# Kernel tuning notes

Hardware: AMD Instinct MI355X
Metric: run time of the kernel (lower is better)

## Reference

```python
import jax, jax.numpy as jnp
import numpy as np

B, N, F_IN, H, OUT = 64, 1024, 195, 128, 64
K1, K2 = N // 2, N // 4  # ceil(0.5*N), ceil(0.5*K1)
EPS = 1e-5


def setup_inputs() -> dict:
    key = jax.random.key(0)
    ks = jax.random.split(key, 16)
    rn = lambda k, s: jax.random.normal(k, s, dtype=jnp.float32) * 0.1
    inp = {
        "input": jax.random.normal(ks[0], (B, N, F_IN), dtype=jnp.float32),
        # SAGEConv1 (195->128): lin_l (neighbors, w/ bias), lin_r (root, no bias)
        "W1l": rn(ks[1], (H, F_IN)), "b1l": jnp.zeros((H,), jnp.float32),
        "W1r": rn(ks[2], (H, F_IN)),
        # SAGPooling1 GNN = GraphConv(128->1): lin_rel (sum aggr, w/ bias), lin_root (no bias)
        "Wp1_rel": rn(ks[3], (1, H)), "bp1_rel": jnp.zeros((1,), jnp.float32),
        "Wp1_root": rn(ks[4], (1, H)),
        # SAGEConv2 (128->64)
        "W2l": rn(ks[5], (OUT, H)), "b2l": jnp.zeros((OUT,), jnp.float32),
        "W2r": rn(ks[6], (OUT, H)),
        # SAGPooling2 GNN = GraphConv(64->1)
        "Wp2_rel": rn(ks[7], (1, OUT)), "bp2_rel": jnp.zeros((1,), jnp.float32),
        "Wp2_root": rn(ks[8], (1, OUT)),
        # MLP head
        "fc1_w": rn(ks[9], (512, OUT)), "fc1_b": jnp.zeros((512,), jnp.float32),
        "bn1_g": jnp.ones((512,), jnp.float32), "bn1_b": jnp.zeros((512,), jnp.float32),
        "bn1_m": jnp.zeros((512,), jnp.float32), "bn1_v": jnp.ones((512,), jnp.float32),
        "fc2_w": rn(ks[10], (256, 512)), "fc2_b": jnp.zeros((256,), jnp.float32),
        "bn2_g": jnp.ones((256,), jnp.float32), "bn2_b": jnp.zeros((256,), jnp.float32),
        "bn2_m": jnp.zeros((256,), jnp.float32), "bn2_v": jnp.ones((256,), jnp.float32),
        "fc3_w": rn(ks[11], (2, 256)), "fc3_b": jnp.zeros((2,), jnp.float32),
    }
    return inp


def _corr_adj(x):
    # Pearson corrcoef over rows of x [B,N,F] -> boolean adjacency [B,N,N] (corr > 0.5)
    xc = x - x.mean(axis=-1, keepdims=True)
    cov = jnp.einsum("bnf,bmf->bnm", xc, xc)
    d = jnp.sqrt(jnp.clip(jnp.einsum("bnnf->bn", cov[..., None] * 0 + 0) + jnp.diagonal(cov, axis1=1, axis2=2), 1e-12))
    corr = cov / (d[:, :, None] * d[:, None, :])
    return (corr > 0.5).astype(x.dtype)  # symmetric, includes self-loops


def _sage(x, A, Wl, bl, Wr):
    # PyG SAGEConv: lin_l(mean_{j in N(i)} x_j) + lin_r(x_i)
    deg = A.sum(axis=-1, keepdims=True)
    agg = jnp.einsum("bnm,bmf->bnf", A, x) / jnp.maximum(deg, 1.0)
    return jnp.einsum("bnf,hf->bnh", agg, Wl) + bl + jnp.einsum("bnf,hf->bnh", x, Wr)


def _sagpool(x, A, Wrel, brel, Wroot, k):
    # score via GraphConv (sum aggr): lin_rel(sum_j x_j) + lin_root(x_i)
    agg = jnp.einsum("bnm,bmf->bnf", A, x)
    score = (jnp.einsum("bnf,of->bno", agg, Wrel) + brel
             + jnp.einsum("bnf,of->bno", x, Wroot))[..., 0]  # [B,N]
    top_s, idx = jax.lax.top_k(score, k)  # per-graph top-k nodes
    x_new = jnp.take_along_axis(x, idx[:, :, None], axis=1) * jnp.tanh(top_s)[:, :, None]
    A_new = jnp.take_along_axis(A, idx[:, :, None], axis=1)
    A_new = jnp.take_along_axis(A_new, idx[:, None, :], axis=2)
    return x_new, A_new


def _bn_eval(x, g, b, m, v):
    return g * (x - m) * jax.lax.rsqrt(v + EPS) + b


def reference(input, W1l, b1l, W1r, Wp1_rel, bp1_rel, Wp1_root,
              W2l, b2l, W2r, Wp2_rel, bp2_rel, Wp2_root,
              fc1_w, fc1_b, bn1_g, bn1_b, bn1_m, bn1_v,
              fc2_w, fc2_b, bn2_g, bn2_b, bn2_m, bn2_v,
              fc3_w, fc3_b):
    A = _corr_adj(input)                                   # [B,N,N]
    x = jax.nn.relu(_sage(input, A, W1l, b1l, W1r))        # [B,N,128]
    x, A = _sagpool(x, A, Wp1_rel, bp1_rel, Wp1_root, K1)  # [B,K1,128]
    x = jax.nn.relu(_sage(x, A, W2l, b2l, W2r))            # [B,K1,64]
    x, A = _sagpool(x, A, Wp2_rel, bp2_rel, Wp2_root, K2)  # [B,K2,64]
    x = x.mean(axis=1)                                     # global mean pool -> [B,64]
    x = _bn_eval(jax.nn.relu(x @ fc1_w.T + fc1_b), bn1_g, bn1_b, bn1_m, bn1_v)
    x = _bn_eval(jax.nn.relu(x @ fc2_w.T + fc2_b), bn2_g, bn2_b, bn2_m, bn2_v)
    x = x @ fc3_w.T + fc3_b
    return jax.nn.softmax(x, axis=1)
```

## Files before the change

### kernel.cpp

```cpp
#include <hip/hip_runtime.h>
#include <hip/hip_fp8.h>
#include <cstdint>


typedef __bf16 bf16x8 __attribute__((ext_vector_type(8)));
typedef float  floatx4 __attribute__((ext_vector_type(4)));

#define MFMA_BF16(a, b, c) __builtin_amdgcn_mfma_f32_16x16x32_bf16((a), (b), (c), 0, 0, 0)
#define MFMA_FP8(a, b, c)  __builtin_amdgcn_mfma_f32_16x16x32_fp8_fp8((a), (b), (c), 0, 0, 0)

typedef __attribute__((address_space(1))) const void as1_cvoid;
typedef __attribute__((address_space(3))) void as3_void;
static __device__ __forceinline__ void gl16(const void* g, void* l) {
  __builtin_amdgcn_global_load_lds((as1_cvoid*)g, (as3_void*)l, 16, 0, 0);
}

static constexpr int BATCH = 64, NNODE = 1024, FIN = 195, FPAD = 224;
static constexpr int HD = 128, OD = 64, KP1 = 512, KP2 = 256;

static constexpr size_t OFF_GHI   = 0;
static constexpr size_t OFF_GLO   = 8388608;
static constexpr size_t OFF_A1B   = 16777216;
static constexpr size_t OFF_YR2   = 18874368;
static constexpr size_t OFF_X2    = 35651584;
static constexpr size_t OFF_XHI   = 0;
static constexpr size_t OFF_XLO   = 29360128;
static constexpr size_t OFF_ABITS = 58720256;
static constexpr size_t OFF_X1    = 67108864;
static constexpr size_t OFF_P1    = 100663296;
static constexpr size_t OFF_Q1    = OFF_P1 + 262144;
static constexpr size_t OFF_IDX1  = OFF_Q1 + 262144;
static constexpr size_t OFF_GATE1 = OFF_IDX1 + 131072;
static constexpr size_t OFF_P2    = OFF_GATE1 + 131072;
static constexpr size_t OFF_Q2    = OFF_P2 + 131072;
static constexpr size_t OFF_W1HI  = OFF_Q2 + 131072;
static constexpr size_t OFF_W1LO  = OFF_W1HI + 114688;
static constexpr size_t OFF_W2HI  = OFF_W1LO + 114688;
static constexpr size_t OFF_W2LO  = OFF_W2HI + 32768;
static constexpr size_t OFF_FC1T  = OFF_W2LO + 32768;
static constexpr size_t OFF_FC2T  = OFF_FC1T + 131072;
static constexpr size_t OFF_XHAT  = 102760448;
static constexpr size_t OFF_YR1   = 102760448 + 16777216;

static __device__ __forceinline__ unsigned char to_fp8(float v) {
  __hip_fp8_e4m3 q(v);
  return *(unsigned char*)&q;
}

__global__ __launch_bounds__(256) void prep_pack_kernel(
    const float* __restrict__ x, __bf16* __restrict__ xhi,
    __bf16* __restrict__ xlo, unsigned char* __restrict__ xhat8,
    const float* __restrict__ W1l, const float* __restrict__ W1r,
    __bf16* __restrict__ hi1, __bf16* __restrict__ lo1,
    const float* __restrict__ W2l, const float* __restrict__ W2r,
    __bf16* __restrict__ hi2, __bf16* __restrict__ lo2,
    const float* __restrict__ fc1w, float* __restrict__ fc1t,
    const float* __restrict__ fc2w, float* __restrict__ fc2t) {
  int bid = blockIdx.x;
  if (bid < 16384) {
    int row  = bid * 4 + (threadIdx.x >> 6);
    int lane = threadIdx.x & 63;
    const float* xr = x + (long)row * FIN;
    int k0 = lane * 4;
    float v[4];
#pragma unroll
    for (int i = 0; i < 4; ++i) v[i] = (k0 + i < FIN) ? xr[k0 + i] : 0.f;
    float s = v[0] + v[1] + v[2] + v[3];
#pragma unroll
    for (int o = 32; o; o >>= 1) s += __shfl_xor(s, o);
    float mean = s * (1.f / (float)FIN);
    float c[4], ss = 0.f;
#pragma unroll
    for (int i = 0; i < 4; ++i) {
      c[i] = (k0 + i < FIN) ? (v[i] - mean) : 0.f;
      ss += c[i] * c[i];
    }
#pragma unroll
    for (int o = 32; o; o >>= 1) ss += __shfl_xor(ss, o);
    float inv = rsqrtf(fmaxf(ss, 1e-12f));
    if (k0 < FPAD) {
      __bf16 hi4[4], lo4[4];
      unsigned char h8[4];
#pragma unroll
      for (int i = 0; i < 4; ++i) {
        float xv = (k0 + i < FIN) ? v[i] : 0.f;
        __bf16 h = (__bf16)xv;
        hi4[i] = h;
        lo4[i] = (__bf16)(xv - (float)h);
        h8[i] = to_fp8(c[i] * inv);
      }
      long base = (long)row * FPAD + k0;
      *(uint2*)&xhi[base] = *(const uint2*)hi4;
      *(uint2*)&xlo[base] = *(const uint2*)lo4;
      *(unsigned int*)&xhat8[base] = *(const unsigned int*)h8;
    }
  } else if (bid < 16384 + 224) {
    int idx = (bid - 16384) * 256 + threadIdx.x;
    int h = idx / FPAD, k = idx % FPAD;
    float v = 0.f;
    if (k < FIN) v = (h < HD) ? W1l[h * FIN + k] : W1r[(h - HD) * FIN + k];
    __bf16 a = (__bf16)v;
    hi1[idx] = a;
    lo1[idx] = (__bf16)(v - (float)a);
  } else if (bid < 16672) {
    int idx = (bid - 16384 - 224) * 256 + threadIdx.x;
    int h = idx / HD, k = idx % HD;
    float v = (h < OD) ? W2l[h * HD + k] : W2r[(h - OD) * HD + k];
    __bf16 a = (__bf16)v;
    hi2[idx] = a;
    lo2[idx] = (__bf16)(v - (float)a);
  } else if (bid < 16800) {
    int idx = (bid - 16672) * 256 + threadIdx.x;
    int o = idx & 511, j = idx >> 9;
    fc1t[idx] = fc1w[o * 64 + j];
  } else {
    int idx = (bid - 16800) * 256 + threadIdx.x;
    int o = idx & 255, j = idx >> 8;
    fc2t[idx] = fc2w[o * 512 + j];
  }
}

static constexpr int CKB = 48;
__global__ __launch_bounds__(256, 3) void corr_gemm1_kernel(
    const unsigned char* __restrict__ xhat8, unsigned short* __restrict__ Abits,
    const __bf16* __restrict__ Ahi, const __bf16* __restrict__ Alo,
    const __bf16* __restrict__ Bhi, const __bf16* __restrict__ Blo,
    float* __restrict__ C) {
  __shared__ __align__(16) char pool[32768];
  int bid = blockIdx.x;
  int t = threadIdx.x;
  int lane = t & 63, wave = t >> 6;
  int wi = (wave >> 1) * 64, wj = (wave & 1) * 64;
  int lr = lane & 15;
  if (bid < 2304) {
    unsigned char* sI = (unsigned char*)pool;
    unsigned char* sJ = (unsigned char*)pool + 2 * 128 * CKB;
    int xcd = bid & 7;
    int m = bid >> 3;
    int b = xcd + ((m & 7) << 3);
    int rem = m >> 3, bi = 0;
    while (rem >= 8 - bi) { rem -= 8 - bi; ++bi; }
    int bj = bi + rem;
    int i0 = bi * 128, j0 = bj * 128;
    const unsigned char* Xb = xhat8 + (long)b * NNODE * FPAD;
    int lk8 = (lane >> 4) * 8;
    int strow = t & 127;
    int sbuf = t >> 7;
    const unsigned char* src = Xb + (long)((sbuf ? j0 : i0) + strow) * FPAD;
    unsigned char* dst0 = (sbuf ? sJ : sI) + strow * CKB;
    floatx4 zero = {0.f, 0.f, 0.f, 0.f};
    floatx4 acc[4][4];
#pragma unroll
    for (int i = 0; i < 4; ++i)
#pragma unroll
      for (int j = 0; j < 4; ++j) acc[i][j] = zero;
    {
      uint4 u0 = *(const uint4*)(src);
      uint4 u1 = *(const uint4*)(src + 16);
      *(uint4*)(dst0)      = u0;
      *(uint4*)(dst0 + 16) = u1;
    }
    __syncthreads();
    for (int kk = 0; kk < 7; ++kk) {
      int cur = kk & 1;
      uint4 u0, u1;
      if (kk < 6) {
        const unsigned char* s2 = src + (kk + 1) * 32;
        u0 = *(const uint4*)(s2);
        u1 = *(const uint4*)(s2 + 16);
      }
      const unsigned char* rI = sI + cur * (128 * CKB);
      const unsigned char* rJ = sJ + cur * (128 * CKB);
      long long af[4], bf[4];
#pragma unroll
      for (int tt = 0; tt < 4; ++tt) {
        af[tt] = *(const long long*)&rI[(wi + tt * 16 + lr) * CKB + lk8];
        bf[tt] = *(const long long*)&rJ[(wj + tt * 16 + lr) * CKB + lk8];
      }
#pragma unroll
      for (int ti = 0; ti < 4; ++ti)
#pragma unroll
        for (int tj = 0; tj < 4; ++tj)
          acc[ti][tj] = MFMA_FP8(af[ti], bf[tj], acc[ti][tj]);
      if (kk < 6) {
        unsigned char* d = dst0 + (cur ? 0 : 128 * CKB);
        *(uint4*)(d)      = u0;
        *(uint4*)(d + 16) = u1;
        __syncthreads();
      }
    }
#pragma unroll
    for (int ti = 0; ti < 4; ++ti)
#pragma unroll
      for (int tj = 0; tj < 4; ++tj) {
        floatx4 a = acc[ti][tj];
        unsigned long long mr[4];
        mr[0] = __ballot(a[0] > 0.5f);
        mr[1] = __ballot(a[1] > 0.5f);
        mr[2] = __ballot(a[2] > 0.5f);
        mr[3] = __ballot(a[3] > 0.5f);
        if (lane < 16) {
          unsigned long long mm = mr[lane & 3];
          unsigned short piece = (unsigned short)(mm >> ((lane >> 2) * 16));
          int grow = i0 + wi + ti * 16 + lane;
          int gcol = (j0 + wj + tj * 16) >> 4;
          Abits[((long)b * NNODE + grow) * 64 + gcol] = piece;
          if (bi != bj) {
            unsigned int tp = 0;
#pragma unroll
            for (int tb = 0; tb < 16; ++tb)
              tp |= (unsigned int)((mr[tb & 3] >> ((tb >> 2) * 16 + lane)) & 1ULL) << tb;
            int grow2 = j0 + wj + tj * 16 + lane;
            int gcol2 = (i0 + wi + ti * 16) >> 4;
            Abits[((long)b * NNODE + grow2) * 64 + gcol2] = (unsigned short)tp;
          }
        }
      }
  } else {
    constexpr int K = 224;
    constexpr int ldc = 256;
    int gid = bid - 2304;
    int xcd = gid & 7;
    int q = gid >> 3;
    int col = q & 1;
    int mrow = (xcd << 6) + (q >> 1);
    __bf16* sAh = (__bf16*)pool;
    __bf16* sAl = (__bf16*)(pool + 8192);
    __bf16* sBh = (__bf16*)(pool + 16384);
    __bf16* sBl = (__bf16*)(pool + 24576);
    long row0 = (long)mrow * 128;
    int col0 = col * 128;
    int lk2 = (lane >> 4) * 16;
    int lk2s = lk2 ^ (((lr >> 1) & 3) << 4);
    int sr = t >> 2;
    int scb = (((t & 3) ^ ((sr >> 1) & 3)) << 4);
    const char* gA0 = (const char*)Ahi + (row0 + sr) * (long)K * 2 + scb;
    const char* gA1 = (const char*)Alo + (row0 + sr) * (long)K * 2 + scb;
    const char* gB0 = (const char*)Bhi + (long)(col0 + sr) * K * 2 + scb;
    const char* gB1 = (const char*)Blo + (long)(col0 + sr) * K * 2 + scb;
    constexpr long rstep = 64L * K * 2;
    char* lAh = (char*)sAh + (wave << 10);
    char* lAl = (char*)sAl + (wave << 10);
    char* lBh = (char*)sBh + (wave << 10);
    char* lBl = (char*)sBl + (wave << 10);
    floatx4 zero = {0.f, 0.f, 0.f, 0.f};
    floatx4 acc[4][4];
#pragma unroll
    for (int i = 0; i < 4; ++i)
#pragma unroll
      for (int j = 0; j < 4; ++j) acc[i][j] = zero;
    for (int kk = 0; kk < (K >> 5); ++kk) {
      __syncthreads();
      gl16(gA0, lAh); gl16(gA0 + rstep, lAh + 4096);
      gl16(gA1, lAl); gl16(gA1 + rstep, lAl + 4096);
      gl16(gB0, lBh); gl16(gB0 + rstep, lBh + 4096);
      gl16(gB1, lBl); gl16(gB1 + rstep, lBl + 4096);
      gA0 += 64; gA1 += 64; gB0 += 64; gB1 += 64;
      __syncthreads();
      bf16x8 bh[4], bl[4];
#pragma unroll
      for (int tj = 0; tj < 4; ++tj) {
        bh[tj] = *(const bf16x8*)((const char*)sBh + (wj + tj * 16 + lr) * 64 + lk2s);
        bl[tj] = *(const bf16x8*)((const char*)sBl + (wj + tj * 16 + lr) * 64 + lk2s);
      }
#pragma unroll
      for (int ti = 0; ti < 4; ++ti) {
        bf16x8 ah = *(const bf16x8*)((const char*)sAh + (wi + ti * 16 + lr) * 64 + lk2s);
        bf16x8 al = *(const bf16x8*)((const char*)sAl + (wi + ti * 16 + lr) * 64 + lk2s);
#pragma unroll
        for (int tj = 0; tj < 4; ++tj) acc[ti][tj] = MFMA_BF16(ah, bh[tj], acc[ti][tj]);
#pragma unroll
        for (int tj = 0; tj < 4; ++tj) acc[ti][tj] = MFMA_BF16(ah, bl[tj], acc[ti][tj]);
#pragma unroll
        for (int tj = 0; tj < 4; ++tj) acc[ti][tj] = MFMA_BF16(al, bh[tj], acc[ti][tj]);
      }
    }
#pragma unroll
    for (int ti = 0; ti < 4; ++ti)
#pragma unroll
      for (int tj = 0; tj < 4; ++tj)
#pragma unroll
        for (int rr = 0; rr < 4; ++rr) {
          long grow = row0 + wi + ti * 16 + (lane >> 4) * 4 + rr;
          int gcol = col0 + wj + tj * 16 + (lane & 15);
          C[grow * ldc + gcol] = acc[ti][tj][rr];
        }
  }
}

template <int K, int NCOL>
__global__ __launch_bounds__(256, 3) void gemm_split_kernel(
    const __bf16* __restrict__ Ahi, const __bf16* __restrict__ Alo,
    const __bf16* __restrict__ Bhi, const __bf16* __restrict__ Blo,
    float* __restrict__ C) {
  constexpr int ldc = NCOL * 128;
  int bid = blockIdx.x;
  int mrow, col;
  if (NCOL == 2) {
    int xcd = bid & 7;
    int q = bid >> 3;
    col = q & 1;
    mrow = (xcd << 6) + (q >> 1);
  } else {
    mrow = bid;
    col = 0;
  }
  __shared__ __align__(16) __bf16 sAh[128 * 32];
  __shared__ __align__(16) __bf16 sAl[128 * 32];
  __shared__ __align__(16) __bf16 sBh[128 * 32];
  __shared__ __align__(16) __bf16 sBl[128 * 32];
  long row0 = (long)mrow * 128;
  int col0 = col * 128;
  int t = threadIdx.x;
  int lane = t & 63, wave = t >> 6;
  int wi = (wave >> 1) * 64, wj = (wave & 1) * 64;
  int lr = lane & 15, lk2 = (lane >> 4) * 16;
  int lk2s = lk2 ^ (((lr >> 1) & 3) << 4);
  int sr = t >> 2;
  int scb = (((t & 3) ^ ((sr >> 1) & 3)) << 4);
  const char* gA0 = (const char*)Ahi + (row0 + sr) * (long)K * 2 + scb;
  const char* gA1 = (const char*)Alo + (row0 + sr) * (long)K * 2 + scb;
  const char* gB0 = (const char*)Bhi + (long)(col0 + sr) * K * 2 + scb;
  const char* gB1 = (const char*)Blo + (long)(col0 + sr) * K * 2 + scb;
  constexpr long rstep = 64L * K * 2;
  char* lAh = (char*)sAh + (wave << 10);
  char* lAl = (char*)sAl + (wave << 10);
  char* lBh = (char*)sBh + (wave << 10);
  char* lBl = (char*)sBl + (wave << 10);
  floatx4 zero = {0.f, 0.f, 0.f, 0.f};
  floatx4 acc[4][4];
#pragma unroll
  for (int i = 0; i < 4; ++i)
#pragma unroll
    for (int j = 0; j < 4; ++j) acc[i][j] = zero;
  for (int kk = 0; kk < (K >> 5); ++kk) {
    __syncthreads();
    gl16(gA0, lAh); gl16(gA0 + rstep, lAh + 4096);
    gl16(gA1, lAl); gl16(gA1 + rstep, lAl + 4096);
    gl16(gB0, lBh); gl16(gB0 + rstep, lBh + 4096);
    gl16(gB1, lBl); gl16(gB1 + rstep, lBl + 4096);
    gA0 += 64; gA1 += 64; gB0 += 64; gB1 += 64;
    __syncthreads();
    bf16x8 bh[4], bl[4];
#pragma unroll
    for (int tj = 0; tj < 4; ++tj) {
      bh[tj] = *(const bf16x8*)((const char*)sBh + (wj + tj * 16 + lr) * 64 + lk2s);
      bl[tj] = *(const bf16x8*)((const char*)sBl + (wj + tj * 16 + lr) * 64 + lk2s);
    }
#pragma unroll
    for (int ti = 0; ti < 4; ++ti) {
      bf16x8 ah = *(const bf16x8*)((const char*)sAh + (wi + ti * 16 + lr) * 64 + lk2s);
      bf16x8 al = *(const bf16x8*)((const char*)sAl + (wi + ti * 16 + lr) * 64 + lk2s);
#pragma unroll
      for (int tj = 0; tj < 4; ++tj) acc[ti][tj] = MFMA_BF16(ah, bh[tj], acc[ti][tj]);
#pragma unroll
      for (int tj = 0; tj < 4; ++tj) acc[ti][tj] = MFMA_BF16(ah, bl[tj], acc[ti][tj]);
#pragma unroll
      for (int tj = 0; tj < 4; ++tj) acc[ti][tj] = MFMA_BF16(al, bh[tj], acc[ti][tj]);
    }
  }
#pragma unroll
  for (int ti = 0; ti < 4; ++ti)
#pragma unroll
    for (int tj = 0; tj < 4; ++tj)
#pragma unroll
      for (int rr = 0; rr < 4; ++rr) {
        long grow = row0 + wi + ti * 16 + (lane >> 4) * 4 + rr;
        int gcol = col0 + wj + tj * 16 + (lane & 15);
        C[grow * ldc + gcol] = acc[ti][tj][rr];
      }
}

__global__ __launch_bounds__(256) void sage1_kernel(
    const unsigned int* __restrict__ Abits32, const float* __restrict__ YR1,
    const float* __restrict__ b1l, const float* __restrict__ Wrel,
    const float* __restrict__ Wroot, float* __restrict__ x1,
    float* __restrict__ p1, float* __restrict__ q1) {
  int g = threadIdx.x >> 5;
  int lane = threadIdx.x & 31;
  int node = blockIdx.x * 8 + g;
  int b = node >> 10, nloc = node & 1023;
  __shared__ int list[8][1024];
  __shared__ int s_deg[8];
  {
    unsigned int word = Abits32[(long)node * 32 + lane];
    int cnt = __popc(word);
    int off = cnt;
#pragma unroll
    for (int o = 1; o < 32; o <<= 1) {
      int v = __shfl_up(off, o, 32);
      if (lane >= o) off += v;
    }
    off -= cnt;
    if (lane == 31) s_deg[g] = off + cnt;
    int basei = lane * 32;
    while (word) {
      int t = __ffs(word) - 1;
      word &= word - 1;
      list[g][off++] = basei + t;
    }
  }
  __syncthreads();
  int deg = s_deg[g];
  const float4* Y4 = (const float4*)(YR1 + (long)(b << 10) * 256);
  float4 a4 = {0.f, 0.f, 0.f, 0.f};
  for (int d = 0; d < deg; ++d) {
    float4 y = Y4[(long)list[g][d] * 64 + lane];
    a4.x += y.x; a4.y += y.y; a4.z += y.z; a4.w += y.w;
  }
  float4 R = Y4[(long)nloc * 64 + 32 + lane];
  float inv = 1.f / (float)(deg < 1 ? 1 : deg);
  float4 bl = ((const float4*)b1l)[lane];
  float4 v;
  v.x = fmaxf(a4.x * inv + bl.x + R.x, 0.f);
  v.y = fmaxf(a4.y * inv + bl.y + R.y, 0.f);
  v.z = fmaxf(a4.z * inv + bl.z + R.z, 0.f);
  v.w = fmaxf(a4.w * inv + bl.w + R.w, 0.f);
  ((float4*)x1)[(long)node * 32 + lane] = v;
  float4 wr = ((const float4*)Wrel)[lane];
  float4 wq = ((const float4*)Wroot)[lane];
  float pv = v.x * wr.x + v.y * wr.y + v.z * wr.z + v.w * wr.w;
  float qv = v.x * wq.x + v.y * wq.y + v.z * wq.z + v.w * wq.w;
#pragma unroll
  for (int o = 16; o; o >>= 1) {
    pv += __shfl_xor(pv, o, 32);
    qv += __shfl_xor(qv, o, 32);
  }
  if (lane == 0) { p1[node] = pv; q1[node] = qv; }
}

__global__ void scoretopk_kernel(const unsigned int* __restrict__ bits32,
                                 const float* __restrict__ p,
                                 const float* __restrict__ q,
                                 const float* __restrict__ brel,
                                 int* __restrict__ idx_out,
                                 float* __restrict__ gate_out,
                                 int nwords, int rpb_shift, int k) {
  int b = blockIdx.x, tid = threadIdx.x;
  int row = (b << rpb_shift) + tid;
  const unsigned int* wptr = bits32 + (long)row * nwords;
  const float* pb = p + ((long)b << rpb_shift);
  float s = q[row] + brel[0];
  for (int w = 0; w < nwords; ++w) {
    unsigned int word = wptr[w];
    while (word) {
      int t = __ffs(word) - 1;
      word &= word - 1;
      s += pb[w * 32 + t];
    }
  }
  unsigned int fb = __float_as_uint(s);
  unsigned int key = (fb & 0x80000000u) ? ~fb : (fb | 0x80000000u);
  __shared__ int hist[256];
  __shared__ unsigned int sh_prefix;
  __shared__ int sh_target, cnt_gt, cnt_eq, outpos;
  if (tid == 0) { sh_prefix = 0; sh_target = k; cnt_gt = 0; cnt_eq = 0; outpos = 0; }
  for (int shift = 24; shift >= 0; shift -= 8) {
    if (tid < 256) hist[tid] = 0;
    __syncthreads();
    unsigned int prefix = sh_prefix;
    bool inset = (shift == 24) || ((key >> (shift + 8)) == (prefix >> (shift + 8)));
    if (inset) atomicAdd(&hist[(key >> shift) & 255], 1);
    __syncthreads();
    if (tid < 64) {
      int lane = tid;
      int bb0 = hist[255 - 4 * lane];
      int bb1 = hist[254 - 4 * lane];
      int bb2 = hist[253 - 4 * lane];
      int bb3 = hist[252 - 4 * lane];
      int c0 = bb0, c1 = c0 + bb1, c2 = c1 + bb2, c3 = c2 + bb3;
      int incl = c3;
#pragma unroll
      for (int o = 1; o < 64; o <<= 1) {
        int v = __shfl_up(incl, o);
        if (lane >= o) incl += v;
      }
      int excl = incl - c3;
      int target = sh_target;
      int cum[4] = {excl + c0, excl + c1, excl + c2, excl + c3};
      int prev = excl;
#pragma unroll
      for (int i = 0; i < 4; ++i) {
        if (cum[i] >= target && prev < target) {
          int bin = 255 - (4 * lane + i);
          sh_prefix = prefix | ((unsigned int)bin << shift);
          sh_target = target - prev;
        }
        prev = cum[i];
      }
    }
    __syncthreads();
  }
  unsigned int T = sh_prefix;
  if (key > T) atomicAdd(&cnt_gt, 1);
  __syncthreads();
  int E = k - cnt_gt;
  bool sel = (key > T);
  if (!sel && key == T) sel = (atomicAdd(&cnt_eq, 1) < E);
  if (sel) {
    int posn = atomicAdd(&outpos, 1);
    idx_out[b * k + posn] = tid;
    gate_out[b * k + posn] = tanhf(s);
  }
}

__global__ __launch_bounds__(256) void gather_kernel(
    const float* __restrict__ x1, const int* __restrict__ idx,
    const float* __restrict__ gate, __bf16* __restrict__ ghi,
    __bf16* __restrict__ glo, const unsigned int* __restrict__ Abits32,
    unsigned long long* __restrict__ A1bits) {
  int bid = blockIdx.x;
  if (bid < 16384) {
    long e = (long)bid * 256 + threadIdx.x;
    int h = (int)(e & 127);
    int i = (int)((e >> 7) & 511);
    int b = (int)(e >> 16);
    int srow = idx[(b << 9) + i];
    float v = x1[((long)(b << 10) + srow) * 128 + h] * gate[(b << 9) + i];
    __bf16 a = (__bf16)v;
    ghi[e] = a;
    glo[e] = (__bf16)(v - (float)a);
  } else {
    int gi = (bid - 16384) * 4 + (threadIdx.x >> 6);
    int lane = threadIdx.x & 63;
    int b = gi >> 9;
    int srow = idx[gi];
    const unsigned int* src = Abits32 + ((long)(b << 10) + srow) * 32;
    const int* idxb = idx + (b << 9);
#pragma unroll
    for (int t = 0; t < 8; ++t) {
      int cj = idxb[t * 64 + lane];
      int bit = (src[cj >> 5] >> (cj & 31)) & 1;
      unsigned long long m = __ballot(bit);
      if (lane == 0) A1bits[(long)gi * 8 + t] = m;
    }
  }
}

__global__ __launch_bounds__(256) void sage2_kernel(
    const unsigned int* __restrict__ A1b32, const float* __restrict__ YR2,
    const float* __restrict__ b2l, const float* __restrict__ Wrel,
    const float* __restrict__ Wroot, float* __restrict__ x2,
    float* __restrict__ p2, float* __restrict__ q2) {
  int g = threadIdx.x >> 4;
  int lane = threadIdx.x & 15;
  int row = blockIdx.x * 16 + g;
  int b = row >> 9, iloc = row & 511;
  __shared__ int list[16][512];
  __shared__ int s_deg[16];
  {
    unsigned int word = A1b32[(long)row * 16 + lane];
    int cnt = __popc(word);
    int off = cnt;
#pragma unroll
    for (int o = 1; o < 16; o <<= 1) {
      int v = __shfl_up(off, o, 16);
      if (lane >= o) off += v;
    }
    off -= cnt;
    if (lane == 15) s_deg[g] = off + cnt;
    int basei = lane * 32;
    while (word) {
      int t = __ffs(word) - 1;
      word &= word - 1;
      list[g][off++] = basei + t;
    }
  }
  __syncthreads();
  int deg = s_deg[g];
  const float4* Y4 = (const float4*)(YR2 + (long)(b << 9) * 128);
  float4 a4 = {0.f, 0.f, 0.f, 0.f};
  for (int d = 0; d < deg; ++d) {
    float4 y = Y4[(long)list[g][d] * 32 + lane];
    a4.x += y.x; a4.y += y.y; a4.z += y.z; a4.w += y.w;
  }
  float4 R = Y4[(long)iloc * 32 + 16 + lane];
  float inv = 1.f / (float)(deg < 1 ? 1 : deg);
  float4 bl = ((const float4*)b2l)[lane];
  float4 v;
  v.x = fmaxf(a4.x * inv + bl.x + R.x, 0.f);
  v.y = fmaxf(a4.y * inv + bl.y + R.y, 0.f);
  v.z = fmaxf(a4.z * inv + bl.z + R.z, 0.f);
  v.w = fmaxf(a4.w * inv + bl.w + R.w, 0.f);
  ((float4*)x2)[(long)row * 16 + lane] = v;
  float4 wr = ((const float4*)Wrel)[lane];
  float4 wq = ((const float4*)Wroot)[lane];
  float pv = v.x * wr.x + v.y * wr.y + v.z * wr.z + v.w * wr.w;
  float qv = v.x * wq.x + v.y * wq.y + v.z * wq.z + v.w * wq.w;
#pragma unroll
  for (int o = 8; o; o >>= 1) {
    pv += __shfl_xor(pv, o, 16);
    qv += __shfl_xor(qv, o, 16);
  }
  if (lane == 0) { p2[row] = pv; q2[row] = qv; }
}

__global__ __launch_bounds__(512) void scoretopk_head_kernel(
    const unsigned int* __restrict__ A1b32, const float* __restrict__ p2,
    const float* __restrict__ q2, const float* __restrict__ brel,
    const float* __restrict__ x2, const float* __restrict__ fc1t,
    const float* __restrict__ fc1_b, const float* __restrict__ g1,
    const float* __restrict__ bb1, const float* __restrict__ m1,
    const float* __restrict__ v1, const float* __restrict__ fc2t,
    const float* __restrict__ fc2_b, const float* __restrict__ g2,
    const float* __restrict__ bb2, const float* __restrict__ m2,
    const float* __restrict__ v2, const float* __restrict__ fc3_w,
    const float* __restrict__ fc3_b, float* __restrict__ out) {
  int b = blockIdx.x, tid = threadIdx.x;
  int row = (b << 9) + tid;
  const unsigned int* wptr = A1b32 + (long)row * 16;
  const float* pb = p2 + ((long)b << 9);
  float s = q2[row] + brel[0];
  for (int w = 0; w < 16; ++w) {
    unsigned int word = wptr[w];
    while (word) {
      int t = __ffs(word) - 1;
      word &= word - 1;
      s += pb[w * 32 + t];
    }
  }
  constexpr int k = KP2;
  unsigned int fb = __float_as_uint(s);
  unsigned int key = (fb & 0x80000000u) ? ~fb : (fb | 0x80000000u);
  __shared__ int hist[256];
  __shared__ int idx2s[256];
  __shared__ float gate2s[256];
  __shared__ unsigned int sh_prefix;
  __shared__ int sh_target, cnt_gt, cnt_eq, outpos;
  if (tid == 0) { sh_prefix = 0; sh_target = k; cnt_gt = 0; cnt_eq = 0; outpos = 0; }
  for (int shift = 24; shift >= 0; shift -= 8) {
    if (tid < 256) hist[tid] = 0;
    __syncthreads();
    unsigned int prefix = sh_prefix;
    bool inset = (shift == 24) || ((key >> (shift + 8)) == (prefix >> (shift + 8)));
    if (inset) atomicAdd(&hist[(key >> shift) & 255], 1);
    __syncthreads();
    if (tid < 64) {
      int lane = tid;
      int bb0 = hist[255 - 4 * lane];
      int bb1 = hist[254 - 4 * lane];
      int bb2 = hist[253 - 4 * lane];
      int bb3 = hist[252 - 4 * lane];
      int c0 = bb0, c1 = c0 + bb1, c2 = c1 + bb2, c3 = c2 + bb3;
      int incl = c3;
#pragma unroll
      for (int o = 1; o < 64; o <<= 1) {
        int v = __shfl_up(incl, o);
        if (lane >= o) incl += v;
      }
      int excl = incl - c3;
      int target = sh_target;
      int cum[4] = {excl + c0, excl + c1, excl + c2, excl + c3};
      int prev = excl;
#pragma unroll
      for (int i = 0; i < 4; ++i) {
        if (cum[i] >= target && prev < target) {
          int bin = 255 - (4 * lane + i);
          sh_prefix = prefix | ((unsigned int)bin << shift);
          sh_target = target - prev;
        }
        prev = cum[i];
      }
    }
    __syncthreads();
  }
  unsigned int T = sh_prefix;
  if (key > T) atomicAdd(&cnt_gt, 1);
  __syncthreads();
  int E = k - cnt_gt;
  bool sel = (key > T);
  if (!sel && key == T) sel = (atomicAdd(&cnt_eq, 1) < E);
  if (sel) {
    int posn = atomicAdd(&outpos, 1);
    idx2s[posn] = tid;
    gate2s[posn] = tanhf(s);
  }
  __syncthreads();
  __shared__ float part[8][64];
  __shared__ float pooled[64];
  __shared__ float h1[512];
  __shared__ float h2[256];
  __shared__ float zz[2];
  int h = tid & 63, grp = tid >> 6;
  float sp = 0.f;
  for (int i = grp * 32; i < grp * 32 + 32; ++i) {
    int si = idx2s[i];
    sp += x2[((long)(b << 9) + si) * 64 + h] * gate2s[i];
  }
  part[grp][h] = sp;
  __syncthreads();
  if (tid < 64) {
    float t = 0.f;
#pragma unroll
    for (int g = 0; g < 8; ++g) t += part[g][tid];
    pooled[tid] = t * (1.f / 256.f);
  }
  __syncthreads();
  {
    float z = fc1_b[tid];
#pragma unroll 8
    for (int j = 0; j < 64; ++j) z += pooled[j] * fc1t[j * 512 + tid];
    z = fmaxf(z, 0.f);
    h1[tid] = g1[tid] * (z - m1[tid]) * rsqrtf(v1[tid] + 1e-5f) + bb1[tid];
  }
  __syncthreads();
  if (tid < 256) {
    float z = fc2_b[tid];
#pragma unroll 8
    for (int j = 0; j < 512; ++j) z += h1[j] * fc2t[j * 256 + tid];
    z = fmaxf(z, 0.f);
    h2[tid] = g2[tid] * (z - m2[tid]) * rsqrtf(v2[tid] + 1e-5f) + bb2[tid];
  }
  __syncthreads();
  if (tid < 2) {
    float z = fc3_b[tid];
    for (int j = 0; j < 256; ++j) z += h2[j] * fc3_w[tid * 256 + j];
    zz[tid] = z;
  }
  __syncthreads();
  if (tid == 0) {
    float mx = fmaxf(zz[0], zz[1]);
    float e0 = expf(zz[0] - mx), e1 = expf(zz[1] - mx);
    float inv = 1.f / (e0 + e1);
    out[b * 2 + 0] = e0 * inv;
    out[b * 2 + 1] = e1 * inv;
  }
}

extern "C" void kernel_launch(void* const* d_in, const int* in_sizes, int n_in,
                              void* d_out, int out_size, void* d_ws, size_t ws_size,
                              hipStream_t stream) {
  (void)in_sizes; (void)n_in; (void)out_size; (void)ws_size;
  const float* input   = (const float*)d_in[0];
  const float* W1l     = (const float*)d_in[1];
  const float* b1l     = (const float*)d_in[2];
  const float* W1r     = (const float*)d_in[3];
  const float* Wp1_rel = (const float*)d_in[4];
  const float* bp1_rel = (const float*)d_in[5];
  const float* Wp1_root= (const float*)d_in[6];
  const float* W2l     = (const float*)d_in[7];
  const float* b2l     = (const float*)d_in[8];
  const float* W2r     = (const float*)d_in[9];
  const float* Wp2_rel = (const float*)d_in[10];
  const float* bp2_rel = (const float*)d_in[11];
  const float* Wp2_root= (const float*)d_in[12];
  const float* fc1_w   = (const float*)d_in[13];
  const float* fc1_b   = (const float*)d_in[14];
  const float* bn1_g   = (const float*)d_in[15];
  const float* bn1_b   = (const float*)d_in[16];
  const float* bn1_m   = (const float*)d_in[17];
  const float* bn1_v   = (const float*)d_in[18];
  const float* fc2_w   = (const float*)d_in[19];
  const float* fc2_b   = (const float*)d_in[20];
  const float* bn2_g   = (const float*)d_in[21];
  const float* bn2_b   = (const float*)d_in[22];
  const float* bn2_m   = (const float*)d_in[23];
  const float* bn2_v   = (const float*)d_in[24];
  const float* fc3_w   = (const float*)d_in[25];
  const float* fc3_b   = (const float*)d_in[26];

  char* ws = (char*)d_ws;
  __bf16* xhi   = (__bf16*)(ws + OFF_XHI);
  __bf16* xlo   = (__bf16*)(ws + OFF_XLO);
  unsigned char* xhat8 = (unsigned char*)(ws + OFF_XHAT);
  unsigned short* Abits = (unsigned short*)(ws + OFF_ABITS);
  const unsigned int* Abits32 = (const unsigned int*)(ws + OFF_ABITS);
  float* YR1    = (float*)(ws + OFF_YR1);
  float* x1     = (float*)(ws + OFF_X1);
  float* p1     = (float*)(ws + OFF_P1);
  float* q1     = (float*)(ws + OFF_Q1);
  int*   idx1   = (int*)(ws + OFF_IDX1);
  float* gate1  = (float*)(ws + OFF_GATE1);
  float* p2     = (float*)(ws + OFF_P2);
  float* q2     = (float*)(ws + OFF_Q2);
  __bf16* w1hi  = (__bf16*)(ws + OFF_W1HI);
  __bf16* w1lo  = (__bf16*)(ws + OFF_W1LO);
  __bf16* w2hi  = (__bf16*)(ws + OFF_W2HI);
  __bf16* w2lo  = (__bf16*)(ws + OFF_W2LO);
  float* fc1t   = (float*)(ws + OFF_FC1T);
  float* fc2t   = (float*)(ws + OFF_FC2T);
  __bf16* ghi   = (__bf16*)(ws + OFF_GHI);
  __bf16* glo   = (__bf16*)(ws + OFF_GLO);
  unsigned long long* A1bits = (unsigned long long*)(ws + OFF_A1B);
  const unsigned int* A1b32  = (const unsigned int*)(ws + OFF_A1B);
  float* YR2    = (float*)(ws + OFF_YR2);
  float* x2     = (float*)(ws + OFF_X2);
  float* out    = (float*)d_out;

  prep_pack_kernel<<<17312, 256, 0, stream>>>(input, xhi, xlo, xhat8,
                                              W1l, W1r, w1hi, w1lo,
                                              W2l, W2r, w2hi, w2lo,
                                              fc1_w, fc1t, fc2_w, fc2t);
  corr_gemm1_kernel<<<3328, 256, 0, stream>>>(xhat8, Abits,
                                              xhi, xlo, w1hi, w1lo, YR1);
  sage1_kernel<<<8192, 256, 0, stream>>>(Abits32, YR1, b1l, Wp1_rel, Wp1_root, x1, p1, q1);
  scoretopk_kernel<<<64, 1024, 0, stream>>>(Abits32, p1, q1, bp1_rel, idx1, gate1,
                                            32, 10, KP1);
  gather_kernel<<<24576, 256, 0, stream>>>(x1, idx1, gate1, ghi, glo, Abits32, A1bits);
  gemm_split_kernel<128, 1><<<256, 256, 0, stream>>>(
      ghi, glo, w2hi, w2lo, YR2);
  sage2_kernel<<<2048, 256, 0, stream>>>(A1b32, YR2, b2l, Wp2_rel, Wp2_root, x2, p2, q2);
  scoretopk_head_kernel<<<64, 512, 0, stream>>>(A1b32, p2, q2, bp2_rel, x2,
                                                fc1t, fc1_b, bn1_g, bn1_b, bn1_m, bn1_v,
                                                fc2t, fc2_b, bn2_g, bn2_b, bn2_m, bn2_v,
                                                fc3_w, fc3_b, out);
}
```

Baseline: 322.4 us.

## Register-prefetch next K tile in split-bf16 GEMMs instead of direct global-to-LDS loads

Replaces the global_load_lds direct-to-LDS copies in both split-bf16 GEMM kernels with register-staged loads. Each iteration prefetches the next K tile into registers while the MFMAs run on the current tile, then writes it to LDS between barriers. The aim is to hide global load latency behind compute, which the old load-then-sync-then-compute loop exposed. The cost is eight extra uint4 registers per thread, which may reduce occupancy, plus extra VGPR-to-LDS store instructions.

```diff
diff --git a/kernel.cpp b/kernel.cpp
--- a/kernel.cpp
+++ b/kernel.cpp
@@ -8,12 +8,6 @@
 
 #define MFMA_BF16(a, b, c) __builtin_amdgcn_mfma_f32_16x16x32_bf16((a), (b), (c), 0, 0, 0)
 #define MFMA_FP8(a, b, c)  __builtin_amdgcn_mfma_f32_16x16x32_fp8_fp8((a), (b), (c), 0, 0, 0)
-
-typedef __attribute__((address_space(1))) const void as1_cvoid;
-typedef __attribute__((address_space(3))) void as3_void;
-static __device__ __forceinline__ void gl16(const void* g, void* l) {
-  __builtin_amdgcn_global_load_lds((as1_cvoid*)g, (as3_void*)l, 16, 0, 0);
-}
 
 static constexpr int BATCH = 64, NNODE = 1024, FIN = 195, FPAD = 224;
 static constexpr int HD = 128, OD = 64, KP1 = 512, KP2 = 256;
@@ -239,24 +233,36 @@
     const char* gB0 = (const char*)Bhi + (long)(col0 + sr) * K * 2 + scb;
     const char* gB1 = (const char*)Blo + (long)(col0 + sr) * K * 2 + scb;
     constexpr long rstep = 64L * K * 2;
-    char* lAh = (char*)sAh + (wave << 10);
-    char* lAl = (char*)sAl + (wave << 10);
-    char* lBh = (char*)sBh + (wave << 10);
-    char* lBl = (char*)sBl + (wave << 10);
+    char* dAh = (char*)sAh + t * 16;
+    char* dAl = (char*)sAl + t * 16;
+    char* dBh = (char*)sBh + t * 16;
+    char* dBl = (char*)sBl + t * 16;
     floatx4 zero = {0.f, 0.f, 0.f, 0.f};
     floatx4 acc[4][4];
 #pragma unroll
     for (int i = 0; i < 4; ++i)
 #pragma unroll
       for (int j = 0; j < 4; ++j) acc[i][j] = zero;
+    {
+      uint4 a0 = *(const uint4*)(gA0), a1 = *(const uint4*)(gA0 + rstep);
+      uint4 b0 = *(const uint4*)(gA1), b1 = *(const uint4*)(gA1 + rstep);
+      uint4 c0 = *(const uint4*)(gB0), c1 = *(const uint4*)(gB0 + rstep);
+      uint4 d0 = *(const uint4*)(gB1), d1 = *(const uint4*)(gB1 + rstep);
+      *(uint4*)dAh = a0; *(uint4*)(dAh + 4096) = a1;
+      *(uint4*)dAl = b0; *(uint4*)(dAl + 4096) = b1;
+      *(uint4*)dBh = c0; *(uint4*)(dBh + 4096) = c1;
+      *(uint4*)dBl = d0; *(uint4*)(dBl + 4096) = d1;
+    }
+    __syncthreads();
     for (int kk = 0; kk < (K >> 5); ++kk) {
-      __syncthreads();
-      gl16(gA0, lAh); gl16(gA0 + rstep, lAh + 4096);
-      gl16(gA1, lAl); gl16(gA1 + rstep, lAl + 4096);
-      gl16(gB0, lBh); gl16(gB0 + rstep, lBh + 4096);
-      gl16(gB1, lBl); gl16(gB1 + rstep, lBl + 4096);
-      gA0 += 64; gA1 += 64; gB0 += 64; gB1 += 64;
-      __syncthreads();
+      uint4 a0, a1, b0, b1, c0, c1, d0, d1;
+      if (kk + 1 < (K >> 5)) {
+        long ko = (long)(kk + 1) * 64;
+        a0 = *(const uint4*)(gA0 + ko); a1 = *(const uint4*)(gA0 + ko + rstep);
+        b0 = *(const uint4*)(gA1 + ko); b1 = *(const uint4*)(gA1 + ko + rstep);
+        c0 = *(const uint4*)(gB0 + ko); c1 = *(const uint4*)(gB0 + ko + rstep);
+        d0 = *(const uint4*)(gB1 + ko); d1 = *(const uint4*)(gB1 + ko + rstep);
+      }
       bf16x8 bh[4], bl[4];
 #pragma unroll
       for (int tj = 0; tj < 4; ++tj) {
@@ -273,6 +279,14 @@
         for (int tj = 0; tj < 4; ++tj) acc[ti][tj] = MFMA_BF16(ah, bl[tj], acc[ti][tj]);
 #pragma unroll
         for (int tj = 0; tj < 4; ++tj) acc[ti][tj] = MFMA_BF16(al, bh[tj], acc[ti][tj]);
+      }
+      if (kk + 1 < (K >> 5)) {
+        __syncthreads();
+        *(uint4*)dAh = a0; *(uint4*)(dAh + 4096) = a1;
+        *(uint4*)dAl = b0; *(uint4*)(dAl + 4096) = b1;
+        *(uint4*)dBh = c0; *(uint4*)(dBh + 4096) = c1;
+        *(uint4*)dBl = d0; *(uint4*)(dBl + 4096) = d1;
+        __syncthreads();
       }
     }
 #pragma unroll
@@ -323,24 +337,36 @@
   const char* gB0 = (const char*)Bhi + (long)(col0 + sr) * K * 2 + scb;
   const char* gB1 = (const char*)Blo + (long)(col0 + sr) * K * 2 + scb;
   constexpr long rstep = 64L * K * 2;
-  char* lAh = (char*)sAh + (wave << 10);
-  char* lAl = (char*)sAl + (wave << 10);
-  char* lBh = (char*)sBh + (wave << 10);
-  char* lBl = (char*)sBl + (wave << 10);
+  char* dAh = (char*)sAh + t * 16;
+  char* dAl = (char*)sAl + t * 16;
+  char* dBh = (char*)sBh + t * 16;
+  char* dBl = (char*)sBl + t * 16;
   floatx4 zero = {0.f, 0.f, 0.f, 0.f};
   floatx4 acc[4][4];
 #pragma unroll
   for (int i = 0; i < 4; ++i)
 #pragma unroll
     for (int j = 0; j < 4; ++j) acc[i][j] = zero;
+  {
+    uint4 a0 = *(const uint4*)(gA0), a1 = *(const uint4*)(gA0 + rstep);
+    uint4 b0 = *(const uint4*)(gA1), b1 = *(const uint4*)(gA1 + rstep);
+    uint4 c0 = *(const uint4*)(gB0), c1 = *(const uint4*)(gB0 + rstep);
+    uint4 d0 = *(const uint4*)(gB1), d1 = *(const uint4*)(gB1 + rstep);
+    *(uint4*)dAh = a0; *(uint4*)(dAh + 4096) = a1;
+    *(uint4*)dAl = b0; *(uint4*)(dAl + 4096) = b1;
+    *(uint4*)dBh = c0; *(uint4*)(dBh + 4096) = c1;
+    *(uint4*)dBl = d0; *(uint4*)(dBl + 4096) = d1;
+  }
+  __syncthreads();
   for (int kk = 0; kk < (K >> 5); ++kk) {
-    __syncthreads();
-    gl16(gA0, lAh); gl16(gA0 + rstep, lAh + 4096);
-    gl16(gA1, lAl); gl16(gA1 + rstep, lAl + 4096);
-    gl16(gB0, lBh); gl16(gB0 + rstep, lBh + 4096);
-    gl16(gB1, lBl); gl16(gB1 + rstep, lBl + 4096);
-    gA0 += 64; gA1 += 64; gB0 += 64; gB1 += 64;
-    __syncthreads();
+    uint4 a0, a1, b0, b1, c0, c1, d0, d1;
+    if (kk + 1 < (K >> 5)) {
+      long ko = (long)(kk + 1) * 64;
+      a0 = *(const uint4*)(gA0 + ko); a1 = *(const uint4*)(gA0 + ko + rstep);
+      b0 = *(const uint4*)(gA1 + ko); b1 = *(const uint4*)(gA1 + ko + rstep);
+      c0 = *(const uint4*)(gB0 + ko); c1 = *(const uint4*)(gB0 + ko + rstep);
+      d0 = *(const uint4*)(gB1 + ko); d1 = *(const uint4*)(gB1 + ko + rstep);
+    }
     bf16x8 bh[4], bl[4];
 #pragma unroll
     for (int tj = 0; tj < 4; ++tj) {
@@ -357,6 +383,14 @@
       for (int tj = 0; tj < 4; ++tj) acc[ti][tj] = MFMA_BF16(ah, bl[tj], acc[ti][tj]);
 #pragma unroll
       for (int tj = 0; tj < 4; ++tj) acc[ti][tj] = MFMA_BF16(al, bh[tj], acc[ti][tj]);
+    }
+    if (kk + 1 < (K >> 5)) {
+      __syncthreads();
+      *(uint4*)dAh = a0; *(uint4*)(dAh + 4096) = a1;
+      *(uint4*)dAl = b0; *(uint4*)(dAl + 4096) = b1;
+      *(uint4*)dBh = c0; *(uint4*)(dBh + 4096) = c1;
+      *(uint4*)dBl = d0; *(uint4*)(dBl + 4096) = d1;
+      __syncthreads();
     }
   }
 #pragma unroll
```

Measured after the change: 322.8 us. No clear change (+0.1%).
